# Performance work log

Measured on AMD Instinct MI355X. Metric: run time of the kernel, lower is better.

## Reference

```python
import jax, jax.numpy as jnp
import numpy as np

N = 10000      # nodes
E0 = 100000    # edges (no self loops); self loops appended -> E = E0 + N
IN = 512       # input feature dim
HID = 256      # out_channels per head
OUT = 10       # classes
H1, H2 = 4, 1  # heads conv1 / conv2
K = 5          # mixture-of-Gaussians prior components ('mixGau-5')
ON = 2 * HID   # out_neurons per head (mean | raw-std)
D1, D2 = H1 * HID, H2 * HID  # latent dims per conv
LOG2PI = float(np.log(2.0 * np.pi))


def _norm_logprob(z, mu, sigma):
    return -0.5 * jnp.square((z - mu) / sigma) - jnp.log(sigma) - 0.5 * LOG2PI


def _seg_softmax(logits, seg, n):
    # numerically stable softmax over segments defined by seg (target node ids)
    m = jax.ops.segment_max(logits, seg, num_segments=n)
    e = jnp.exp(logits - m[seg])
    s = jax.ops.segment_sum(e, seg, num_segments=n)
    return e / (s[seg] + 1e-16)


def _gib_conv(x, W, att, pi, mu, logsig, eps, gumbel, src, dst, heads):
    n = x.shape[0]
    xh = (x @ W).reshape(n, heads, ON)                       # [n,H,ON]
    # GAT attention: score(e) = leaky_relu(<x_i,att_l> + <x_j,att_r>)
    s_i = jnp.einsum('nhd,hd->nh', xh, att[:, :ON])
    s_j = jnp.einsum('nhd,hd->nh', xh, att[:, ON:])
    alpha = jax.nn.leaky_relu(s_i[dst] + s_j[src], 0.2)      # [E,H]
    alpha = _seg_softmax(alpha, dst, n)
    # structure KL vs uniform prior 1/deg
    deg = jax.ops.segment_sum(jnp.ones_like(alpha[:, 0]), dst, num_segments=n)
    prior = (1.0 / deg)[dst][:, None]
    kl = (alpha * (jnp.log(alpha + 1e-12) - jnp.log(prior + 1e-12))).sum() / alpha.size
    # categorical structural sampling: gumbel-softmax per segment
    alpha_s = _seg_softmax(jnp.log(alpha + 1e-16) + gumbel, dst, n)
    out = jax.ops.segment_sum(xh[src] * alpha_s[:, :, None], dst, num_segments=n)  # [n,H,ON]
    # per-head diag reparameterization: ON = (mean:HID | raw std:HID)
    mean = out[..., :HID].reshape(n, heads * HID)
    std = jax.nn.softplus(out[..., HID:]).reshape(n, heads * HID) + 1e-10
    Z = mean[None] + std[None] * eps                         # [S,n,D]
    log_q = _norm_logprob(Z, mean[None], std[None]).sum(-1)  # [S,n]
    # mixture-of-Gaussians feature prior, per-dimension mixture
    logpi = jax.nn.log_softmax(pi)
    comp = _norm_logprob(Z[..., None], mu, jnp.exp(logsig)) + logpi  # [S,n,D,K]
    prior_lp = jax.nn.logsumexp(comp, axis=-1).sum(-1)       # [S,n]
    ixz = (log_q - prior_lp).mean()
    return Z.mean(0), kl, ixz


def setup_inputs() -> dict:
    key = jax.random.key(0)
    ks = jax.random.split(key, 20)
    x = jax.random.normal(ks[0], (N, IN), jnp.float32)
    # edge list guaranteed free of self-loops (remove_self_loops is then a no-op)
    s = jax.random.randint(ks[1], (E0,), 0, N)
    off = jax.random.randint(ks[2], (E0,), 1, N)
    edge_index = jnp.stack([s, (s + off) % N]).astype(jnp.int32)
    E = E0 + N

    def xav(k, fi, fo):
        a = np.sqrt(6.0 / (fi + fo)).astype(np.float32)
        return jax.random.uniform(k, (fi, fo), jnp.float32, -a, a)

    def gumbel(k, shape):
        u = jax.random.uniform(k, shape, jnp.float32, 1e-6, 1.0 - 1e-6)
        return -jnp.log(-jnp.log(u))

    return {
        'x': x, 'edge_index': edge_index,
        'W1': xav(ks[3], IN, H1 * ON),
        'att1': xav(ks[4], H1, 2 * ON),
        'pi1': jnp.zeros((K,), jnp.float32),
        'mu1': jax.random.normal(ks[5], (D1, K), jnp.float32) * 0.1,
        'logsig1': jnp.zeros((D1, K), jnp.float32),
        'eps1': jax.random.normal(ks[6], (1, N, D1), jnp.float32),
        'g1': gumbel(ks[7], (E, H1)),
        'W2': xav(ks[8], D1, H2 * ON),
        'att2': xav(ks[9], H2, 2 * ON),
        'pi2': jnp.zeros((K,), jnp.float32),
        'mu2': jax.random.normal(ks[10], (D2, K), jnp.float32) * 0.1,
        'logsig2': jnp.zeros((D2, K), jnp.float32),
        'eps2': jax.random.normal(ks[11], (1, N, D2), jnp.float32),
        'g2': gumbel(ks[12], (E, H2)),
        'Wfc': xav(ks[13], D2, OUT),
        'bfc': jnp.zeros((OUT,), jnp.float32),
    }


def reference(x, edge_index, W1, att1, pi1, mu1, logsig1, eps1, g1,
              W2, att2, pi2, mu2, logsig2, eps2, g2, Wfc, bfc):
    n = x.shape[0]
    loop = jnp.arange(n, dtype=edge_index.dtype)
    src = jnp.concatenate([edge_index[0], loop])
    dst = jnp.concatenate([edge_index[1], loop])
    h, kl1, ixz1 = _gib_conv(x, W1, att1, pi1, mu1, logsig1, eps1, g1, src, dst, H1)
    h = jax.nn.elu(h)
    h, kl2, ixz2 = _gib_conv(h, W2, att2, pi2, mu2, logsig2, eps2, g2, src, dst, H2)
    h = jax.nn.elu(h)
    logits = h @ Wfc + bfc
    return logits, kl1 + kl2, ixz1 + ixz2
```

## Files before the change

kernel.cpp:

```cpp
#include <hip/hip_runtime.h>
#include <math.h>

constexpr int NN   = 10000;
constexpr int E0C  = 100000;
constexpr int EC   = E0C + NN;
constexpr int INC  = 512;
constexpr int HIDC = 256;
constexpr int OUTC = 10;
constexpr int H1C  = 4;
constexpr int H2C  = 1;
constexpr int ONC  = 2 * HIDC;
constexpr int D1C  = H1C * HIDC;
constexpr int D2C  = H2C * HIDC;
constexpr int KC   = 5;
constexpr float LOG2PI_F = 1.8378770664093453f;

using u16 = unsigned short;
typedef __attribute__((ext_vector_type(8))) short bf16x8;
typedef __attribute__((ext_vector_type(4))) float f32x4;

__device__ __forceinline__ unsigned f2bf(float f) {
    unsigned u = __float_as_uint(f);
    return (u + 0x7fffu + ((u >> 16) & 1u)) >> 16;
}
__device__ __forceinline__ float bflo(unsigned u) { return __uint_as_float(u << 16); }
__device__ __forceinline__ float bfhi(unsigned u) { return __uint_as_float(u & 0xffff0000u); }
__device__ __forceinline__ float bf1(u16 v) { return __uint_as_float(((unsigned)v) << 16); }
__device__ __forceinline__ void edge_sd(int e, const int* __restrict__ ei, int& src, int& dst) {
    if (e < E0C) { src = ei[e]; dst = ei[E0C + e]; }
    else         { src = e - E0C; dst = src; }
}
__device__ __forceinline__ float wmax(float x) {
#pragma unroll
    for (int o = 32; o > 0; o >>= 1) x = fmaxf(x, __shfl_xor(x, o, 64));
    return x;
}
__device__ __forceinline__ float wsum(float x) {
#pragma unroll
    for (int o = 32; o > 0; o >>= 1) x += __shfl_xor(x, o, 64);
    return x;
}

__global__ void zero_u32(unsigned* __restrict__ p, int n) {
    int i = blockIdx.x * blockDim.x + threadIdx.x;
    if (i < n) p[i] = 0u;
}

__global__ void cast_bf16(const float* __restrict__ in, u16* __restrict__ o, int n4) {
    int i = blockIdx.x * blockDim.x + threadIdx.x;
    if (i >= n4) return;
    float4 v = ((const float4*)in)[i];
    uint2 r;
    r.x = f2bf(v.x) | (f2bf(v.y) << 16);
    r.y = f2bf(v.z) | (f2bf(v.w) << 16);
    ((uint2*)o)[i] = r;
}

__global__ __launch_bounds__(256) void transpose_cast_bf16(const float* __restrict__ W,
                                                           u16* __restrict__ WT,
                                                           int K, int N) {
    __shared__ float tile[32][33];
    int n0 = blockIdx.x * 32, k0 = blockIdx.y * 32;
    int tx = threadIdx.x, ty = threadIdx.y;
    for (int r = ty; r < 32; r += 8) tile[r][tx] = W[(size_t)(k0 + r) * N + n0 + tx];
    __syncthreads();
    for (int r = ty; r < 32; r += 8) WT[(size_t)(n0 + r) * K + k0 + tx] = (u16)f2bf(tile[tx][r]);
}

__global__ void count_deg(const int* __restrict__ ei, int* __restrict__ deg) {
    int e = blockIdx.x * blockDim.x + threadIdx.x;
    if (e >= EC) return;
    int dst = (e < E0C) ? ei[E0C + e] : (e - E0C);
    atomicAdd(&deg[dst], 1);
}

__global__ __launch_bounds__(1024) void scan_kernel(const int* __restrict__ deg,
                                                    int* __restrict__ offs) {
    __shared__ int part[1024];
    const int CH = (NN + 1023) / 1024;
    int tid = threadIdx.x;
    int base = tid * CH;
    int s = 0;
    for (int i = 0; i < CH; i++) { int idx = base + i; if (idx < NN) s += deg[idx]; }
    part[tid] = s;
    __syncthreads();
    for (int o = 1; o < 1024; o <<= 1) {
        int v = (tid >= o) ? part[tid - o] : 0;
        __syncthreads();
        part[tid] += v;
        __syncthreads();
    }
    int run = (tid == 0) ? 0 : part[tid - 1];
    for (int i = 0; i < CH; i++) {
        int idx = base + i;
        if (idx < NN) {
            offs[idx] = run;
            run += deg[idx];
        }
    }
    if (tid == 1023) offs[NN] = run;
}

__global__ void csr_fill(const int* __restrict__ ei, int* __restrict__ cursor,
                         const int* __restrict__ offs, int* __restrict__ csr_src,
                         int* __restrict__ csr_eid) {
    int e = blockIdx.x * blockDim.x + threadIdx.x;
    if (e >= EC) return;
    int src, dst;
    edge_sd(e, ei, src, dst);
    int pos = offs[dst] + atomicAdd(&cursor[dst], 1);
    csr_src[pos] = src;
    csr_eid[pos] = e;
}

template <int BM, int BN, int BK, bool BF16OUT>
__global__ __launch_bounds__(256) void mfma_gemm(const u16* __restrict__ A,
                                                 const u16* __restrict__ BT,
                                                 void* __restrict__ Cv,
                                                 int M, int N, int K) {
    constexpr int PK = BK + 16;
    __shared__ __align__(16) u16 As[BM][PK];
    __shared__ __align__(16) u16 Bs[BN][PK];
    const int tid = threadIdx.x;
    const int lane = tid & 63;
    const int wave = tid >> 6;
    const int wm = (wave & 1) * 64;
    const int wn = (wave >> 1) * 64;
    const int row0 = blockIdx.y * BM;
    const int col0 = blockIdx.x * BN;

    f32x4 acc[4][4] = {};
    const int srow = tid >> 1;
    const int shalf = (tid & 1) * 16;
    const int fr = lane & 15;
    const int fq = (lane >> 4) * 8;

    for (int k0 = 0; k0 < K; k0 += BK) {
        uint4 va0 = {0, 0, 0, 0}, va1 = {0, 0, 0, 0};
        int ga = row0 + srow;
        if (ga < M) {
            const uint4* p = (const uint4*)(A + (size_t)ga * K + k0 + shalf);
            va0 = p[0]; va1 = p[1];
        }
        const uint4* pb = (const uint4*)(BT + (size_t)(col0 + srow) * K + k0 + shalf);
        uint4 vb0 = pb[0], vb1 = pb[1];
        __syncthreads();
        *(uint4*)&As[srow][shalf]     = va0;
        *(uint4*)&As[srow][shalf + 8] = va1;
        *(uint4*)&Bs[srow][shalf]     = vb0;
        *(uint4*)&Bs[srow][shalf + 8] = vb1;
        __syncthreads();
        bf16x8 af[4], bfr[4];
#pragma unroll
        for (int i = 0; i < 4; i++) {
            af[i]  = *(const bf16x8*)&As[wm + i * 16 + fr][fq];
            bfr[i] = *(const bf16x8*)&Bs[wn + i * 16 + fr][fq];
        }
#pragma unroll
        for (int mi = 0; mi < 4; mi++)
#pragma unroll
            for (int ni = 0; ni < 4; ni++)
                acc[mi][ni] = __builtin_amdgcn_mfma_f32_16x16x32_bf16(af[mi], bfr[ni], acc[mi][ni], 0, 0, 0);
    }
    const int cc = lane & 15;
    const int cr = (lane >> 4) * 4;
#pragma unroll
    for (int mi = 0; mi < 4; mi++) {
#pragma unroll
        for (int r = 0; r < 4; r++) {
            int grow = row0 + wm + mi * 16 + cr + r;
            if (grow < M) {
#pragma unroll
                for (int ni = 0; ni < 4; ni++) {
                    int gcol = col0 + wn + ni * 16 + cc;
                    if (BF16OUT)
                        ((u16*)Cv)[(size_t)grow * N + gcol] = (u16)f2bf(acc[mi][ni][r]);
                    else
                        ((float*)Cv)[(size_t)grow * N + gcol] = acc[mi][ni][r];
                }
            }
        }
    }
}

template <int H>
__global__ __launch_bounds__(256) void scores_bf16(const u16* __restrict__ xh,
                                                   const float* __restrict__ att,
                                                   float* __restrict__ s_i,
                                                   float* __restrict__ s_j) {
    int gw = (blockIdx.x * 256 + threadIdx.x) >> 6;
    int lane = threadIdx.x & 63;
    if (gw >= NN * H) return;
    int n = gw / H, h = gw - n * H;
    const u16* xr = xh + ((size_t)n * H + h) * ONC;
    uint4 v = ((const uint4*)xr)[lane];
    float xv[8] = { bflo(v.x), bfhi(v.x), bflo(v.y), bfhi(v.y),
                    bflo(v.z), bfhi(v.z), bflo(v.w), bfhi(v.w) };
    const float* base = att + (size_t)h * 2 * ONC;
    const float4* aL = (const float4*)(base + lane * 8);
    const float4* aR = (const float4*)(base + ONC + lane * 8);
    float4 l0 = aL[0], l1 = aL[1], r0 = aR[0], r1 = aR[1];
    float ai = xv[0] * l0.x + xv[1] * l0.y + xv[2] * l0.z + xv[3] * l0.w
             + xv[4] * l1.x + xv[5] * l1.y + xv[6] * l1.z + xv[7] * l1.w;
    float aj = xv[0] * r0.x + xv[1] * r0.y + xv[2] * r0.z + xv[3] * r0.w
             + xv[4] * r1.x + xv[5] * r1.y + xv[6] * r1.z + xv[7] * r1.w;
#pragma unroll
    for (int o = 32; o > 0; o >>= 1) {
        ai += __shfl_down(ai, o, 64);
        aj += __shfl_down(aj, o, 64);
    }
    if (lane == 0) { s_i[gw] = ai; s_j[gw] = aj; }
}

template <int H, int PW>
__global__ __launch_bounds__(256) void attn_fused(const int* __restrict__ offs,
                                                  const int* __restrict__ csr_src,
                                                  const int* __restrict__ csr_eid,
                                                  const float* __restrict__ s_i,
                                                  const float* __restrict__ s_j,
                                                  const float* __restrict__ g,
                                                  float* __restrict__ alpha_csr,
                                                  float* __restrict__ kl_acc,
                                                  float scale) {
    const int tid = threadIdx.x;
    const int wave = tid >> 6, lane = tid & 63;
    const int pair0 = (blockIdx.x * 4 + wave) * PW;
    float kl = 0.f;
#pragma unroll 1
    for (int t = 0; t < PW; t++) {
        int pr = pair0 + t;
        if (pr >= NN * H) break;
        int n = pr / H, h = pr - (pr / H) * H;
        int beg = offs[n], end = offs[n + 1];
        int deg = end - beg;
        float si = s_i[n * H + h];
        float ldeg = __logf((float)deg);
        if (deg <= 64) {
            int pos = beg + lane;
            bool v = lane < deg;
            int src = v ? csr_src[pos] : 0;
            int eid = v ? csr_eid[pos] : 0;
            float a = si + s_j[src * H + h];
            a = (a > 0.f) ? a : 0.2f * a;
            if (!v) a = -3.4e38f;
            float m1 = wmax(a);
            float am = v ? (a - m1) : 0.f;
            float e1 = v ? __expf(am) : 0.f;
            float ss1 = wsum(e1);
            float sd  = wsum(e1 * am);
            float lss1 = __logf(ss1);
            kl += sd / ss1 - lss1 + ldeg;
            float l2 = v ? (am - lss1 + g[eid * H + h]) : -3.4e38f;
            float m2 = wmax(l2);
            float e2 = v ? __expf(l2 - m2) : 0.f;
            float ss2 = wsum(e2);
            if (v) alpha_csr[(size_t)pos * H + h] = e2 / ss2;
        } else {
            float m1 = -3.4e38f;
            for (int p = beg + lane; p < end; p += 64) {
                float a = si + s_j[csr_src[p] * H + h];
                a = (a > 0.f) ? a : 0.2f * a;
                m1 = fmaxf(m1, a);
            }
            m1 = wmax(m1);
            float ss1 = 0.f, sd = 0.f;
            for (int p = beg + lane; p < end; p += 64) {
                float a = si + s_j[csr_src[p] * H + h];
                a = (a > 0.f) ? a : 0.2f * a;
                float e1 = __expf(a - m1);
                ss1 += e1; sd += e1 * (a - m1);
            }
            ss1 = wsum(ss1); sd = wsum(sd);
            float lss1 = __logf(ss1);
            kl += sd / ss1 - lss1 + ldeg;
            float m2 = -3.4e38f;
            for (int p = beg + lane; p < end; p += 64) {
                float a = si + s_j[csr_src[p] * H + h];
                a = (a > 0.f) ? a : 0.2f * a;
                m2 = fmaxf(m2, a - m1 - lss1 + g[csr_eid[p] * H + h]);
            }
            m2 = wmax(m2);
            float ss2 = 0.f;
            for (int p = beg + lane; p < end; p += 64) {
                float a = si + s_j[csr_src[p] * H + h];
                a = (a > 0.f) ? a : 0.2f * a;
                ss2 += __expf(a - m1 - lss1 + g[csr_eid[p] * H + h] - m2);
            }
            ss2 = wsum(ss2);
            for (int p = beg + lane; p < end; p += 64) {
                float a = si + s_j[csr_src[p] * H + h];
                a = (a > 0.f) ? a : 0.2f * a;
                alpha_csr[(size_t)p * H + h] =
                    __expf(a - m1 - lss1 + g[csr_eid[p] * H + h] - m2) / ss2;
            }
        }
    }
    __shared__ float red[4];
    if (lane == 0) red[wave] = kl;
    __syncthreads();
    if (tid == 0)
        atomicAdd(kl_acc, (red[0] + red[1] + red[2] + red[3]) * scale);
}

template <int H, int NP>
__global__ __launch_bounds__(256) void gather_reg2(const u16* __restrict__ xh,
                                                   const float* __restrict__ alpha_csr,
                                                   const int* __restrict__ offs,
                                                   const int* __restrict__ csr_src,
                                                   u16* __restrict__ out) {
    constexpr int ROW = H * ONC;
    constexpr int CPP = ROW / NP;
    constexpr int CL  = CPP / 32;
    const int bx = blockIdx.x;
    const int panel = bx % NP;
    const int wave = threadIdx.x >> 6;
    const int lane = threadIdx.x & 63;
    const int half = lane >> 5;
    const int l32  = lane & 31;
    const int n = (bx / NP) * 8 + wave * 2 + half;
    const int head = (panel * CPP) / ONC;
    const int c0 = panel * CPP + l32 * CL;
    const int beg = offs[n], end = offs[n + 1];
    const int deg = end - beg;
    const int degO = __shfl_xor(deg, 32, 64);
    const int mdeg = max(deg, degO);
    const int bsel = half << 5;
    float acc[CL];
#pragma unroll
    for (int j = 0; j < CL; j++) acc[j] = 0.f;
    for (int c = 0; c < mdeg; c += 32) {
        bool v = (c + l32) < deg;
        int myp = beg + c + l32;
        int   srcv = v ? csr_src[myp] : 0;
        float wv   = v ? alpha_csr[(size_t)myp * H + head] : 0.f;
        int cnt = min(32, mdeg - c);
#pragma unroll 8
        for (int t = 0; t < cnt; t++) {
            int   s = __shfl(srcv, bsel + t, 64);
            float w = __shfl(wv,   bsel + t, 64);
            const u16* xr = xh + (size_t)s * ROW + c0;
            uint4 val = *(const uint4*)xr;
            acc[0] = fmaf(w, bflo(val.x), acc[0]);
            acc[1] = fmaf(w, bfhi(val.x), acc[1]);
            acc[2] = fmaf(w, bflo(val.y), acc[2]);
            acc[3] = fmaf(w, bfhi(val.y), acc[3]);
            acc[4] = fmaf(w, bflo(val.z), acc[4]);
            acc[5] = fmaf(w, bfhi(val.z), acc[5]);
            acc[6] = fmaf(w, bflo(val.w), acc[6]);
            acc[7] = fmaf(w, bfhi(val.w), acc[7]);
        }
    }
    u16* orow = out + (size_t)n * ROW + c0;
    uint4 r;
    r.x = f2bf(acc[0]) | (f2bf(acc[1]) << 16);
    r.y = f2bf(acc[2]) | (f2bf(acc[3]) << 16);
    r.z = f2bf(acc[4]) | (f2bf(acc[5]) << 16);
    r.w = f2bf(acc[6]) | (f2bf(acc[7]) << 16);
    *(uint4*)orow = r;
}

__global__ void mix_table(const float* __restrict__ pi, const float* __restrict__ mu,
                          const float* __restrict__ logsig, float* __restrict__ tab, int DK) {
    int i = blockIdx.x * blockDim.x + threadIdx.x;
    if (i >= DK) return;
    int k = i % KC;
    float p[KC]; float mx = -3.4e38f;
#pragma unroll
    for (int j = 0; j < KC; j++) { p[j] = pi[j]; mx = fmaxf(mx, p[j]); }
    float s = 0.f;
#pragma unroll
    for (int j = 0; j < KC; j++) s += expf(p[j] - mx);
    float lpi = p[k] - (mx + logf(s));
    float ls = logsig[i];
    float inv = expf(-ls);
    float inv2 = inv * inv;
    float m = mu[i];
    tab[i]          = -0.5f * inv2;
    tab[DK + i]     = inv2 * m;
    tab[2 * DK + i] = -0.5f * inv2 * m * m - ls - 0.5f * LOG2PI_F + lpi;
}

template <int NT, bool BF16OUT>
__global__ __launch_bounds__(256) void zixz4_kernel(const u16* __restrict__ in_agg,
                                                    const float* __restrict__ eps,
                                                    const float* __restrict__ tab,
                                                    void* __restrict__ hout_,
                                                    float* __restrict__ ixz_acc) {
    constexpr int H = H1C;
    constexpr int D = H * HIDC;
    constexpr int DK = D * KC;
    const int tid = threadIdx.x;
    const int d0 = tid * 4;
    const int head = d0 >> 8;
    const int c = d0 & 255;
    const int moff = head * ONC + c;
    float ca[4][KC], cb[4][KC], cv[4][KC];
#pragma unroll
    for (int j = 0; j < 4; j++)
#pragma unroll
        for (int k = 0; k < KC; k++) {
            ca[j][k] = tab[(d0 + j) * KC + k];
            cb[j][k] = tab[DK + (d0 + j) * KC + k];
            cv[j][k] = tab[2 * DK + (d0 + j) * KC + k];
        }
    const int n0 = blockIdx.x * NT;
    float local = 0.f;
#pragma unroll 1
    for (int nn = 0; nn < NT; nn++) {
        int n = n0 + nn;
        const u16* orow = in_agg + (size_t)n * (H * ONC);
        uint2 vm = *(const uint2*)(orow + moff);
        uint2 vr = *(const uint2*)(orow + moff + HIDC);
        float4 ep4 = *(const float4*)(eps + (size_t)n * D + d0);
        float mean[4] = { bflo(vm.x), bfhi(vm.x), bflo(vm.y), bfhi(vm.y) };
        float raw[4]  = { bflo(vr.x), bfhi(vr.x), bflo(vr.y), bfhi(vr.y) };
        float epq[4]  = { ep4.x, ep4.y, ep4.z, ep4.w };
        float hv4[4];
#pragma unroll
        for (int j = 0; j < 4; j++) {
            float sp = fmaxf(raw[j], 0.f) + __logf(1.f + __expf(-fabsf(raw[j])));
            float stdv = sp + 1e-10f;
            float ep = epq[j];
            float Z = fmaf(stdv, ep, mean[j]);
            hv4[j] = (Z > 0.f) ? Z : (__expf(Z) - 1.f);
            float logq = fmaf(-0.5f, ep * ep, -__logf(stdv)) - 0.5f * LOG2PI_F;
            float comp[KC]; float mx = -3.4e38f;
#pragma unroll
            for (int k = 0; k < KC; k++) {
                float cval = fmaf(fmaf(ca[j][k], Z, cb[j][k]), Z, cv[j][k]);
                comp[k] = cval;
                mx = fmaxf(mx, cval);
            }
            float se = 0.f;
#pragma unroll
            for (int k = 0; k < KC; k++) se += __expf(comp[k] - mx);
            local += logq - (mx + __logf(se));
        }
        if (BF16OUT) {
            uint2 r;
            r.x = f2bf(hv4[0]) | (f2bf(hv4[1]) << 16);
            r.y = f2bf(hv4[2]) | (f2bf(hv4[3]) << 16);
            *(uint2*)((u16*)hout_ + (size_t)n * D + d0) = r;
        } else {
            *(float4*)((float*)hout_ + (size_t)n * D + d0) =
                make_float4(hv4[0], hv4[1], hv4[2], hv4[3]);
        }
    }
#pragma unroll
    for (int o = 32; o > 0; o >>= 1) local += __shfl_down(local, o, 64);
    __shared__ float red[4];
    int lane = tid & 63, wid = tid >> 6;
    if (lane == 0) red[wid] = local;
    __syncthreads();
    if (tid == 0)
        atomicAdd(ixz_acc, (red[0] + red[1] + red[2] + red[3]) * (1.0f / NN));
}

template <int H, int NT, bool BF16OUT>
__global__ __launch_bounds__(256) void zixz3_kernel(const u16* __restrict__ in_agg,
                                                    const float* __restrict__ eps,
                                                    const float* __restrict__ tab,
                                                    void* __restrict__ hout_,
                                                    float* __restrict__ ixz_acc) {
    constexpr int D = H * HIDC;
    constexpr int DK = D * KC;
    const int tid = threadIdx.x;
    const int h = blockIdx.y;
    const int d = h * HIDC + tid;
    float ca[KC], cb[KC], cc[KC];
#pragma unroll
    for (int k = 0; k < KC; k++) {
        ca[k] = tab[d * KC + k];
        cb[k] = tab[DK + d * KC + k];
        cc[k] = tab[2 * DK + d * KC + k];
    }
    const int n0 = blockIdx.x * NT;
    float local = 0.f;
#pragma unroll 1
    for (int nn = 0; nn < NT; nn++) {
        int n = n0 + nn;
        const u16* orow = in_agg + ((size_t)n * H + h) * ONC;
        float mean = bf1(orow[tid]);
        float raw  = bf1(orow[HIDC + tid]);
        float sp = fmaxf(raw, 0.f) + __logf(1.f + __expf(-fabsf(raw)));
        float stdv = sp + 1e-10f;
        float ep = eps[(size_t)n * D + d];
        float Z = fmaf(stdv, ep, mean);
        float hv = (Z > 0.f) ? Z : (__expf(Z) - 1.f);
        if (BF16OUT) ((u16*)hout_)[(size_t)n * D + d] = (u16)f2bf(hv);
        else         ((float*)hout_)[(size_t)n * D + d] = hv;
        float logq = fmaf(-0.5f, ep * ep, -__logf(stdv)) - 0.5f * LOG2PI_F;
        float comp[KC]; float mx = -3.4e38f;
#pragma unroll
        for (int k = 0; k < KC; k++) {
            float cval = fmaf(fmaf(ca[k], Z, cb[k]), Z, cc[k]);
            comp[k] = cval;
            mx = fmaxf(mx, cval);
        }
        float se = 0.f;
#pragma unroll
        for (int k = 0; k < KC; k++) se += __expf(comp[k] - mx);
        local += logq - (mx + __logf(se));
    }
#pragma unroll
    for (int o = 32; o > 0; o >>= 1) local += __shfl_down(local, o, 64);
    __shared__ float red[4];
    int lane = tid & 63, wid = tid >> 6;
    if (lane == 0) red[wid] = local;
    __syncthreads();
    if (tid == 0) {
        atomicAdd(ixz_acc, (red[0] + red[1] + red[2] + red[3]) * (1.0f / NN));
    }
}

__global__ void fc_kernel(const float* __restrict__ h, const float* __restrict__ W,
                          const float* __restrict__ b, float* __restrict__ out) {
    int idx = blockIdx.x * blockDim.x + threadIdx.x;
    if (idx >= NN * OUTC) return;
    int n = idx / OUTC, o = idx - n * OUTC;
    const float* hr = h + (size_t)n * D2C;
    float acc = b[o];
#pragma unroll 8
    for (int c = 0; c < D2C; c++) acc += hr[c] * W[c * OUTC + o];
    out[idx] = acc;
}

extern "C" void kernel_launch(void* const* d_in, const int* in_sizes, int n_in,
                              void* d_out, int out_size, void* d_ws, size_t ws_size,
                              hipStream_t stream) {
    (void)in_sizes; (void)n_in; (void)out_size; (void)ws_size;
    const float* x       = (const float*)d_in[0];
    const int*   ei      = (const int*)d_in[1];
    const float* W1      = (const float*)d_in[2];
    const float* att1    = (const float*)d_in[3];
    const float* pi1     = (const float*)d_in[4];
    const float* mu1     = (const float*)d_in[5];
    const float* logsig1 = (const float*)d_in[6];
    const float* eps1    = (const float*)d_in[7];
    const float* g1      = (const float*)d_in[8];
    const float* W2      = (const float*)d_in[9];
    const float* att2    = (const float*)d_in[10];
    const float* pi2     = (const float*)d_in[11];
    const float* mu2     = (const float*)d_in[12];
    const float* logsig2 = (const float*)d_in[13];
    const float* eps2    = (const float*)d_in[14];
    const float* g2      = (const float*)d_in[15];
    const float* Wfc     = (const float*)d_in[16];
    const float* bfc     = (const float*)d_in[17];
    float* out = (float*)d_out;

    char* ws = (char*)d_ws;
    const size_t szAB = (size_t)NN * 2048 * sizeof(float);
    char* regA = ws;
    char* regB = ws + szAB;
    size_t cur = 2 * szAB;
    auto alloc = [&](size_t bytes) -> char* {
        char* p = ws + cur;
        cur += (bytes + 255) & ~(size_t)255;
        return p;
    };
    float* alphaB   = (float*)alloc((size_t)EC * H1C * sizeof(float));
    float* s_i      = (float*)alloc((size_t)NN * H1C * sizeof(float));
    float* s_j      = (float*)alloc((size_t)NN * H1C * sizeof(float));
    int*   deg_i    = (int*)alloc(NN * sizeof(int));
    int*   offs     = (int*)alloc((NN + 1) * sizeof(int));
    int*   cursor   = (int*)alloc(NN * sizeof(int));
    int*   csr_src  = (int*)alloc(EC * sizeof(int));
    int*   csr_eid  = (int*)alloc(EC * sizeof(int));
    u16*   xb1     = (u16*)alloc((size_t)NN * INC * sizeof(u16));
    u16*   w1t     = (u16*)alloc((size_t)2048 * 512 * sizeof(u16));
    u16*   w2t     = (u16*)alloc((size_t)512 * 1024 * sizeof(u16));
    float* tab1    = (float*)alloc((size_t)3 * D1C * KC * sizeof(float));
    float* tab2    = (float*)alloc((size_t)3 * D2C * KC * sizeof(float));

    u16*   xh1b = (u16*)regA;
    u16*   out1 = (u16*)regB;
    u16*   h1b  = (u16*)regA;
    u16*   xh2b = (u16*)regB;
    u16*   out2 = (u16*)regA;
    float* h2   = (float*)(regB + (size_t)NN * 512 * sizeof(u16));
    float* kl_acc  = out + (size_t)NN * OUTC;
    float* ixz_acc = kl_acc + 1;

    const int ZB = 256;
    zero_u32<<<(NN + ZB - 1) / ZB, ZB, 0, stream>>>((unsigned*)deg_i, NN);
    zero_u32<<<(NN + ZB - 1) / ZB, ZB, 0, stream>>>((unsigned*)cursor, NN);
    zero_u32<<<1, ZB, 0, stream>>>((unsigned*)kl_acc, 2);

    count_deg<<<(EC + ZB - 1) / ZB, ZB, 0, stream>>>(ei, deg_i);
    scan_kernel<<<1, 1024, 0, stream>>>(deg_i, offs);
    csr_fill<<<(EC + ZB - 1) / ZB, ZB, 0, stream>>>(ei, cursor, offs, csr_src, csr_eid);

    cast_bf16<<<(NN * INC / 4 + ZB - 1) / ZB, ZB, 0, stream>>>(x, xb1, NN * INC / 4);
    transpose_cast_bf16<<<dim3(2048 / 32, 512 / 32), dim3(32, 8), 0, stream>>>(W1, w1t, 512, 2048);
    transpose_cast_bf16<<<dim3(512 / 32, 1024 / 32), dim3(32, 8), 0, stream>>>(W2, w2t, 1024, 512);
    mix_table<<<(D1C * KC + ZB - 1) / ZB, ZB, 0, stream>>>(pi1, mu1, logsig1, tab1, D1C * KC);
    mix_table<<<(D2C * KC + ZB - 1) / ZB, ZB, 0, stream>>>(pi2, mu2, logsig2, tab2, D2C * KC);

    const int MG = (NN + 127) / 128;

    mfma_gemm<128, 128, 32, true><<<dim3(2048 / 128, MG), 256, 0, stream>>>(xb1, w1t, xh1b, NN, 2048, 512);
    scores_bf16<H1C><<<(NN * H1C + 3) / 4, 256, 0, stream>>>(xh1b, att1, s_i, s_j);
    attn_fused<H1C, 8><<<(NN * H1C + 31) / 32, 256, 0, stream>>>(offs, csr_src, csr_eid,
                                                                 s_i, s_j, g1, alphaB, kl_acc,
                                                                 1.0f / (float)(EC * H1C));
    gather_reg2<H1C, 8><<<8 * (NN / 8), 256, 0, stream>>>(xh1b, alphaB, offs, csr_src, out1);
    zixz4_kernel<10, true><<<NN / 10, 256, 0, stream>>>(out1, eps1, tab1, (void*)h1b, ixz_acc);

    mfma_gemm<128, 128, 32, true><<<dim3(512 / 128, MG), 256, 0, stream>>>(h1b, w2t, xh2b, NN, 512, 1024);
    scores_bf16<H2C><<<(NN * H2C + 3) / 4, 256, 0, stream>>>(xh2b, att2, s_i, s_j);
    attn_fused<H2C, 8><<<(NN * H2C + 31) / 32, 256, 0, stream>>>(offs, csr_src, csr_eid,
                                                                 s_i, s_j, g2, alphaB, kl_acc,
                                                                 1.0f / (float)(EC * H2C));
    gather_reg2<H2C, 2><<<2 * (NN / 8), 256, 0, stream>>>(xh2b, alphaB, offs, csr_src, out2);
    zixz3_kernel<H2C, 10, false><<<dim3(NN / 10, H2C), 256, 0, stream>>>(out2, eps2, tab2, (void*)h2, ixz_acc);

    fc_kernel<<<(NN * OUTC + ZB - 1) / ZB, ZB, 0, stream>>>(h2, Wfc, bfc, out);
}
```

Baseline: 433.1 us.

## Fuse attention scores into GEMM epilogue, use direct global-to-LDS loads, merge setup kernels

The GEMM now computes the per-head attention dot products in its epilogue from the fp32 accumulators. It reduces them across lanes and atomically adds them into zero-initialised score buffers, so the separate scores kernel and its re-read of the bf16 projection are gone. Tiles are loaded into LDS with global_load_lds, and the row padding is removed, which may add LDS bank conflicts. Several small setup kernels (zeroing, weight transposes, mixture tables) are merged into single launches to cut launch overhead. Scores now come from unrounded accumulators and are summed by float atomics, so the results can vary slightly from run to run.

```diff
diff --git a/kernel.cpp b/kernel.cpp
--- a/kernel.cpp
+++ b/kernel.cpp
@@ -40,10 +40,21 @@
     for (int o = 32; o > 0; o >>= 1) x += __shfl_xor(x, o, 64);
     return x;
 }
-
-__global__ void zero_u32(unsigned* __restrict__ p, int n) {
+__device__ __forceinline__ void gl_lds16(const u16* g, u16* l) {
+    __builtin_amdgcn_global_load_lds(
+        (const __attribute__((address_space(1))) unsigned int*)g,
+        (__attribute__((address_space(3))) unsigned int*)l, 16, 0, 0);
+}
+
+__global__ void init_zero(unsigned* __restrict__ deg, unsigned* __restrict__ cursor,
+                          unsigned* __restrict__ si1, unsigned* __restrict__ sj1,
+                          unsigned* __restrict__ si2, unsigned* __restrict__ sj2,
+                          unsigned* __restrict__ kl) {
     int i = blockIdx.x * blockDim.x + threadIdx.x;
-    if (i < n) p[i] = 0u;
+    if (i < NN) { deg[i] = 0u; cursor[i] = 0u; }
+    if (i < NN * H1C) { si1[i] = 0u; sj1[i] = 0u; }
+    if (i < NN * H2C) { si2[i] = 0u; sj2[i] = 0u; }
+    if (i < 2) kl[i] = 0u;
 }
 
 __global__ void cast_bf16(const float* __restrict__ in, u16* __restrict__ o, int n4) {
@@ -56,11 +67,18 @@
     ((uint2*)o)[i] = r;
 }
 
-__global__ __launch_bounds__(256) void transpose_cast_bf16(const float* __restrict__ W,
-                                                           u16* __restrict__ WT,
-                                                           int K, int N) {
+__global__ __launch_bounds__(256) void transpose_cast_both(const float* __restrict__ W1,
+                                                           u16* __restrict__ WT1,
+                                                           const float* __restrict__ W2,
+                                                           u16* __restrict__ WT2) {
     __shared__ float tile[32][33];
-    int n0 = blockIdx.x * 32, k0 = blockIdx.y * 32;
+    int bx = blockIdx.x, by = blockIdx.y;
+    const float* W; u16* WT; int K, N, n0, k0;
+    if (by < 16) { W = W1; WT = WT1; K = 512;  N = 2048; n0 = bx * 32; k0 = by * 32; }
+    else {
+        if (bx >= 16) return;
+        W = W2; WT = WT2; K = 1024; N = 512;  n0 = bx * 32; k0 = (by - 16) * 32;
+    }
     int tx = threadIdx.x, ty = threadIdx.y;
     for (int r = ty; r < 32; r += 8) tile[r][tx] = W[(size_t)(k0 + r) * N + n0 + tx];
     __syncthreads();
@@ -113,14 +131,17 @@
     csr_eid[pos] = e;
 }
 
-template <int BM, int BN, int BK, bool BF16OUT>
-__global__ __launch_bounds__(256) void mfma_gemm(const u16* __restrict__ A,
-                                                 const u16* __restrict__ BT,
-                                                 void* __restrict__ Cv,
-                                                 int M, int N, int K) {
-    constexpr int PK = BK + 16;
-    __shared__ __align__(16) u16 As[BM][PK];
-    __shared__ __align__(16) u16 Bs[BN][PK];
+template <int H, bool SCORES>
+__global__ __launch_bounds__(256) void mfma_gemm3(const u16* __restrict__ A,
+                                                  const u16* __restrict__ BT,
+                                                  u16* __restrict__ C,
+                                                  const float* __restrict__ att,
+                                                  float* __restrict__ s_i,
+                                                  float* __restrict__ s_j,
+                                                  int M, int N, int K) {
+    constexpr int BM = 128, BN = 128, BK = 32;
+    __shared__ __align__(16) u16 As[BM * BK];
+    __shared__ __align__(16) u16 Bs[BN * BK];
     const int tid = threadIdx.x;
     const int lane = tid & 63;
     const int wave = tid >> 6;
@@ -128,88 +149,85 @@
     const int wn = (wave >> 1) * 64;
     const int row0 = blockIdx.y * BM;
     const int col0 = blockIdx.x * BN;
-
-    f32x4 acc[4][4] = {};
-    const int srow = tid >> 1;
-    const int shalf = (tid & 1) * 16;
     const int fr = lane & 15;
     const int fq = (lane >> 4) * 8;
-
+    const int srow = lane >> 2;
+    const int scol = (lane & 3) * 8;
+    const int aRa = wave * 32 + srow;
+    const int aRb = aRa + 16;
+    const size_t gA0 = (size_t)min(row0 + aRa, M - 1) * K;
+    const size_t gA1 = (size_t)min(row0 + aRb, M - 1) * K;
+    const size_t gB0 = (size_t)(col0 + aRa) * K;
+    const size_t gB1 = (size_t)(col0 + aRb) * K;
+    u16* lA0 = &As[(wave * 32) * BK];
+    u16* lA1 = &As[(wave * 32 + 16) * BK];
+    u16* lB0 = &Bs[(wave * 32) * BK];
+    u16* lB1 = &Bs[(wave * 32 + 16) * BK];
+    f32x4 acc[4][4] = {};
     for (int k0 = 0; k0 < K; k0 += BK) {
-        uint4 va0 = {0, 0, 0, 0}, va1 = {0, 0, 0, 0};
-        int ga = row0 + srow;
-        if (ga < M) {
-            const uint4* p = (const uint4*)(A + (size_t)ga * K + k0 + shalf);
-            va0 = p[0]; va1 = p[1];
-        }
-        const uint4* pb = (const uint4*)(BT + (size_t)(col0 + srow) * K + k0 + shalf);
-        uint4 vb0 = pb[0], vb1 = pb[1];
-        __syncthreads();
-        *(uint4*)&As[srow][shalf]     = va0;
-        *(uint4*)&As[srow][shalf + 8] = va1;
-        *(uint4*)&Bs[srow][shalf]     = vb0;
-        *(uint4*)&Bs[srow][shalf + 8] = vb1;
+        gl_lds16(A + gA0 + k0 + scol, lA0);
+        gl_lds16(A + gA1 + k0 + scol, lA1);
+        gl_lds16(BT + gB0 + k0 + scol, lB0);
+        gl_lds16(BT + gB1 + k0 + scol, lB1);
         __syncthreads();
         bf16x8 af[4], bfr[4];
 #pragma unroll
         for (int i = 0; i < 4; i++) {
-            af[i]  = *(const bf16x8*)&As[wm + i * 16 + fr][fq];
-            bfr[i] = *(const bf16x8*)&Bs[wn + i * 16 + fr][fq];
+            af[i]  = *(const bf16x8*)&As[(wm + i * 16 + fr) * BK + fq];
+            bfr[i] = *(const bf16x8*)&Bs[(wn + i * 16 + fr) * BK + fq];
         }
 #pragma unroll
         for (int mi = 0; mi < 4; mi++)
 #pragma unroll
             for (int ni = 0; ni < 4; ni++)
                 acc[mi][ni] = __builtin_amdgcn_mfma_f32_16x16x32_bf16(af[mi], bfr[ni], acc[mi][ni], 0, 0, 0);
+        __syncthreads();
     }
     const int cc = lane & 15;
     const int cr = (lane >> 4) * 4;
 #pragma unroll
-    for (int mi = 0; mi < 4; mi++) {
+    for (int mi = 0; mi < 4; mi++)
 #pragma unroll
         for (int r = 0; r < 4; r++) {
             int grow = row0 + wm + mi * 16 + cr + r;
             if (grow < M) {
 #pragma unroll
+                for (int ni = 0; ni < 4; ni++)
+                    C[(size_t)grow * N + col0 + wn + ni * 16 + cc] = (u16)f2bf(acc[mi][ni][r]);
+            }
+        }
+    if (SCORES) {
+        const int head = col0 / ONC;
+        const int cb = col0 - head * ONC + wn + cc;
+        float aLv[4], aRv[4];
+#pragma unroll
+        for (int ni = 0; ni < 4; ni++) {
+            aLv[ni] = att[head * 2 * ONC + cb + ni * 16];
+            aRv[ni] = att[head * 2 * ONC + ONC + cb + ni * 16];
+        }
+#pragma unroll
+        for (int mi = 0; mi < 4; mi++)
+#pragma unroll
+            for (int r = 0; r < 4; r++) {
+                float pi_ = 0.f, pj_ = 0.f;
+#pragma unroll
                 for (int ni = 0; ni < 4; ni++) {
-                    int gcol = col0 + wn + ni * 16 + cc;
-                    if (BF16OUT)
-                        ((u16*)Cv)[(size_t)grow * N + gcol] = (u16)f2bf(acc[mi][ni][r]);
-                    else
-                        ((float*)Cv)[(size_t)grow * N + gcol] = acc[mi][ni][r];
+                    float v = acc[mi][ni][r];
+                    pi_ = fmaf(v, aLv[ni], pi_);
+                    pj_ = fmaf(v, aRv[ni], pj_);
                 }
-            }
-        }
-    }
-}
-
-template <int H>
-__global__ __launch_bounds__(256) void scores_bf16(const u16* __restrict__ xh,
-                                                   const float* __restrict__ att,
-                                                   float* __restrict__ s_i,
-                                                   float* __restrict__ s_j) {
-    int gw = (blockIdx.x * 256 + threadIdx.x) >> 6;
-    int lane = threadIdx.x & 63;
-    if (gw >= NN * H) return;
-    int n = gw / H, h = gw - n * H;
-    const u16* xr = xh + ((size_t)n * H + h) * ONC;
-    uint4 v = ((const uint4*)xr)[lane];
-    float xv[8] = { bflo(v.x), bfhi(v.x), bflo(v.y), bfhi(v.y),
-                    bflo(v.z), bfhi(v.z), bflo(v.w), bfhi(v.w) };
-    const float* base = att + (size_t)h * 2 * ONC;
-    const float4* aL = (const float4*)(base + lane * 8);
-    const float4* aR = (const float4*)(base + ONC + lane * 8);
-    float4 l0 = aL[0], l1 = aL[1], r0 = aR[0], r1 = aR[1];
-    float ai = xv[0] * l0.x + xv[1] * l0.y + xv[2] * l0.z + xv[3] * l0.w
-             + xv[4] * l1.x + xv[5] * l1.y + xv[6] * l1.z + xv[7] * l1.w;
-    float aj = xv[0] * r0.x + xv[1] * r0.y + xv[2] * r0.z + xv[3] * r0.w
-             + xv[4] * r1.x + xv[5] * r1.y + xv[6] * r1.z + xv[7] * r1.w;
-#pragma unroll
-    for (int o = 32; o > 0; o >>= 1) {
-        ai += __shfl_down(ai, o, 64);
-        aj += __shfl_down(aj, o, 64);
-    }
-    if (lane == 0) { s_i[gw] = ai; s_j[gw] = aj; }
+#pragma unroll
+                for (int o = 1; o < 16; o <<= 1) {
+                    pi_ += __shfl_xor(pi_, o, 64);
+                    pj_ += __shfl_xor(pj_, o, 64);
+                }
+                int grow = row0 + wm + mi * 16 + cr + r;
+                if (cc == 0 && grow < M) {
+                    atomicAdd(&s_i[grow * H + head], pi_);
+                    atomicAdd(&s_j[grow * H + head], pj_);
+                }
+            }
+    }
 }
 
 template <int H, int PW>
@@ -359,10 +377,9 @@
     *(uint4*)orow = r;
 }
 
-__global__ void mix_table(const float* __restrict__ pi, const float* __restrict__ mu,
-                          const float* __restrict__ logsig, float* __restrict__ tab, int DK) {
-    int i = blockIdx.x * blockDim.x + threadIdx.x;
-    if (i >= DK) return;
+__device__ __forceinline__ void mix_one(const float* __restrict__ pi, const float* __restrict__ mu,
+                                        const float* __restrict__ logsig, float* __restrict__ tab,
+                                        int DK, int i) {
     int k = i % KC;
     float p[KC]; float mx = -3.4e38f;
 #pragma unroll
@@ -378,6 +395,18 @@
     tab[i]          = -0.5f * inv2;
     tab[DK + i]     = inv2 * m;
     tab[2 * DK + i] = -0.5f * inv2 * m * m - ls - 0.5f * LOG2PI_F + lpi;
+}
+
+__global__ void mix_tables(const float* __restrict__ pi1, const float* __restrict__ mu1,
+                           const float* __restrict__ ls1, float* __restrict__ tab1,
+                           const float* __restrict__ pi2, const float* __restrict__ mu2,
+                           const float* __restrict__ ls2, float* __restrict__ tab2) {
+    int i = blockIdx.x * blockDim.x + threadIdx.x;
+    if (i < D1C * KC) mix_one(pi1, mu1, ls1, tab1, D1C * KC, i);
+    else {
+        int j = i - D1C * KC;
+        if (j < D2C * KC) mix_one(pi2, mu2, ls2, tab2, D2C * KC, j);
+    }
 }
 
 template <int NT, bool BF16OUT>
@@ -560,8 +589,10 @@
         return p;
     };
     float* alphaB   = (float*)alloc((size_t)EC * H1C * sizeof(float));
-    float* s_i      = (float*)alloc((size_t)NN * H1C * sizeof(float));
-    float* s_j      = (float*)alloc((size_t)NN * H1C * sizeof(float));
+    float* s_i1     = (float*)alloc((size_t)NN * H1C * sizeof(float));
+    float* s_j1     = (float*)alloc((size_t)NN * H1C * sizeof(float));
+    float* s_i2     = (float*)alloc((size_t)NN * H2C * sizeof(float));
+    float* s_j2     = (float*)alloc((size_t)NN * H2C * sizeof(float));
     int*   deg_i    = (int*)alloc(NN * sizeof(int));
     int*   offs     = (int*)alloc((NN + 1) * sizeof(int));
     int*   cursor   = (int*)alloc(NN * sizeof(int));
@@ -583,34 +614,33 @@
     float* ixz_acc = kl_acc + 1;
 
     const int ZB = 256;
-    zero_u32<<<(NN + ZB - 1) / ZB, ZB, 0, stream>>>((unsigned*)deg_i, NN);
-    zero_u32<<<(NN + ZB - 1) / ZB, ZB, 0, stream>>>((unsigned*)cursor, NN);
-    zero_u32<<<1, ZB, 0, stream>>>((unsigned*)kl_acc, 2);
+    init_zero<<<(NN * H1C + ZB - 1) / ZB, ZB, 0, stream>>>(
+        (unsigned*)deg_i, (unsigned*)cursor, (unsigned*)s_i1, (unsigned*)s_j1,
+        (unsigned*)s_i2, (unsigned*)s_j2, (unsigned*)kl_acc);
 
     count_deg<<<(EC + ZB - 1) / ZB, ZB, 0, stream>>>(ei, deg_i);
     scan_kernel<<<1, 1024, 0, stream>>>(deg_i, offs);
     csr_fill<<<(EC + ZB - 1) / ZB, ZB, 0, stream>>>(ei, cursor, offs, csr_src, csr_eid);
 
     cast_bf16<<<(NN * INC / 4 + ZB - 1) / ZB, ZB, 0, stream>>>(x, xb1, NN * INC / 4);
-    transpose_cast_bf16<<<dim3(2048 / 32, 512 / 32), dim3(32, 8), 0, stream>>>(W1, w1t, 512, 2048);
-    transpose_cast_bf16<<<dim3(512 / 32, 1024 / 32), dim3(32, 8), 0, stream>>>(W2, w2t, 1024, 512);
-    mix_table<<<(D1C * KC + ZB - 1) / ZB, ZB, 0, stream>>>(pi1, mu1, logsig1, tab1, D1C * KC);
-    mix_table<<<(D2C * KC + ZB - 1) / ZB, ZB, 0, stream>>>(pi2, mu2, logsig2, tab2, D2C * KC);
+    transpose_cast_both<<<dim3(64, 48), dim3(32, 8), 0, stream>>>(W1, w1t, W2, w2t);
+    mix_tables<<<((D1C + D2C) * KC + ZB - 1) / ZB, ZB, 0, stream>>>(
+        pi1, mu1, logsig1, tab1, pi2, mu2, logsig2, tab2);
 
     const int MG = (NN + 127) / 128;
 
-    mfma_gemm<128, 128, 32, true><<<dim3(2048 / 128, MG), 256, 0, stream>>>(xb1, w1t, xh1b, NN, 2048, 512);
-    scores_bf16<H1C><<<(NN * H1C + 3) / 4, 256, 0, stream>>>(xh1b, att1, s_i, s_j);
+    mfma_gemm3<H1C, true><<<dim3(2048 / 128, MG), 256, 0, stream>>>(
+        xb1, w1t, xh1b, att1, s_i1, s_j1, NN, 2048, 512);
     attn_fused<H1C, 8><<<(NN * H1C + 31) / 32, 256, 0, stream>>>(offs, csr_src, csr_eid,
-                                                                 s_i, s_j, g1, alphaB, kl_acc,
+                                                                 s_i1, s_j1, g1, alphaB, kl_acc,
                                                                  1.0f / (float)(EC * H1C));
     gather_reg2<H1C, 8><<<8 * (NN / 8), 256, 0, stream>>>(xh1b, alphaB, offs, csr_src, out1);
     zixz4_kernel<10, true><<<NN / 10, 256, 0, stream>>>(out1, eps1, tab1, (void*)h1b, ixz_acc);
 
-    mfma_gemm<128, 128, 32, true><<<dim3(512 / 128, MG), 256, 0, stream>>>(h1b, w2t, xh2b, NN, 512, 1024);
-    scores_bf16<H2C><<<(NN * H2C + 3) / 4, 256, 0, stream>>>(xh2b, att2, s_i, s_j);
+    mfma_gemm3<H2C, true><<<dim3(512 / 128, MG), 256, 0, stream>>>(
+        h1b, w2t, xh2b, att2, s_i2, s_j2, NN, 512, 1024);
     attn_fused<H2C, 8><<<(NN * H2C + 31) / 32, 256, 0, stream>>>(offs, csr_src, csr_eid,
-                                                                 s_i, s_j, g2, alphaB, kl_acc,
+                                                                 s_i2, s_j2, g2, alphaB, kl_acc,
                                                                  1.0f / (float)(EC * H2C));
     gather_reg2<H2C, 2><<<2 * (NN / 8), 256, 0, stream>>>(xh2b, alphaB, offs, csr_src, out2);
     zixz3_kernel<H2C, 10, false><<<dim3(NN / 10, H2C), 256, 0, stream>>>(out2, eps2, tab2, (void*)h2, ixz_acc);
```

New measurement: 462.0 us. 6.7% more time.
